# Optimization experiments

Hardware: AMD Instinct MI355X
Metric: run time of the kernel (lower is better)

Reference implementation:

```python
import jax, jax.numpy as jnp
import numpy as np

N_NODES = 10000
N_EDGES = 640000
N_GRAPHS = 64
IN_FEAT = 128
HID = (128, 128)
NUM_CLASS = 10


def setup_inputs() -> dict:
    key = jax.random.key(0)
    ks = jax.random.split(key, 10)
    x = jax.random.normal(ks[0], (N_NODES, IN_FEAT), dtype=jnp.float32)
    edge_index = jax.random.randint(ks[1], (2, N_EDGES), 0, N_NODES, dtype=jnp.int64)
    batch = jnp.sort(jax.random.randint(ks[2], (N_NODES,), 0, N_GRAPHS, dtype=jnp.int64))
    # GCNConv weights (PyG applies x @ W then propagates, bias added after aggregation)
    s1 = 1.0 / np.sqrt(IN_FEAT)
    s2 = 1.0 / np.sqrt(HID[0])
    s3 = 1.0 / np.sqrt(HID[1])
    W1 = jax.random.uniform(ks[3], (IN_FEAT, HID[0]), jnp.float32, -s1, s1)
    b1 = jnp.zeros((HID[0],), jnp.float32)
    W2 = jax.random.uniform(ks[4], (HID[0], HID[1]), jnp.float32, -s2, s2)
    b2 = jnp.zeros((HID[1],), jnp.float32)
    Wlin = jax.random.uniform(ks[5], (HID[1], NUM_CLASS), jnp.float32, -s3, s3)
    blin = jax.random.uniform(ks[6], (NUM_CLASS,), jnp.float32, -s3, s3)
    return {"x": x, "edge_index": edge_index, "batch": batch,
            "W1": W1, "b1": b1, "W2": W2, "b2": b2, "Wlin": Wlin, "blin": blin}


def _gcn_conv(x, src, dst, W, b):
    # GCNConv with self-loops and symmetric normalization:
    # out[i] = sum_{(j->i) in E} d[j]^{-1/2} d[i]^{-1/2} (x_j W) + d[i]^{-1} (x_i W) + b
    # where d = in-degree (on dst) + 1 for the self-loop.
    h = x @ W                                                      # [N, F]
    ones = jnp.ones(src.shape[0], dtype=h.dtype)
    deg = jax.ops.segment_sum(ones, dst, num_segments=x.shape[0]) + 1.0
    dinv = jax.lax.rsqrt(deg)                                      # [N]
    norm = dinv[src] * dinv[dst]                                   # [E]
    agg = jax.ops.segment_sum(h[src] * norm[:, None], dst, num_segments=x.shape[0])
    agg = agg + h * (dinv * dinv)[:, None]                         # self-loop term
    return agg + b


def _global_mean_pool(x, batch, num_graphs):
    sums = jax.ops.segment_sum(x, batch, num_segments=num_graphs)          # [G, F]
    cnt = jax.ops.segment_sum(jnp.ones(x.shape[0], x.dtype), batch, num_segments=num_graphs)
    return sums / jnp.maximum(cnt, 1.0)[:, None]


def reference(x, edge_index, batch, W1, b1, W2, b2, Wlin, blin):
    src, dst = edge_index[0], edge_index[1]
    h = jax.nn.relu(_gcn_conv(x, src, dst, W1, b1))
    h = jax.nn.relu(_gcn_conv(h, src, dst, W2, b2))
    g = _global_mean_pool(h, batch, N_GRAPHS)      # [G, hid1]
    return g @ Wlin + blin                          # [G, num_class]
```

## Files before the change

kernel.cpp:

```cpp
#include <hip/hip_runtime.h>
#include <hip/hip_bf16.h>

#define NN 10000
#define NE 640000
#define NG 64
#define NF 128
#define NC 10
#define TMR 16
#define TKC 32
#define NB 250
#define BSZ 40
#define G1 512
#define ECHUNK 1250


__device__ __forceinline__ unsigned short f2bf(float f) {
    unsigned int u = __float_as_uint(f);
    return (unsigned short)((u + 0x7FFF + ((u >> 16) & 1)) >> 16);
}
__device__ __forceinline__ float bf_lo(unsigned int p) {
    return __uint_as_float(p << 16);
}
__device__ __forceinline__ float bf_hi(unsigned int p) {
    return __uint_as_float(p & 0xFFFF0000u);
}

__device__ __forceinline__ void scan_btot(const int* __restrict__ btot,
                                          int* bbs, int* vv, int* wsum) {
    int tid = threadIdx.x, lane = tid & 63, wv = tid >> 6;
    int v = (tid < NB) ? btot[tid] : 0;
    vv[tid] = v;
    int p = v;
    for (int o = 1; o < 64; o <<= 1) {
        int t = __shfl_up(p, o, 64);
        if (lane >= o) p += t;
    }
    if (lane == 63) wsum[wv] = p;
    __syncthreads();
    int off = 0;
#pragma unroll
    for (int j = 0; j < 4; ++j) if (j < wv) off += wsum[j];
    bbs[tid] = p + off - v;
    __syncthreads();
}

__device__ __forceinline__ int detect64(const int* w, long span) {
    int lane = threadIdx.x & 63;
    long e = (long)lane * (span - 1) / 63;
    return (__ballot(w[2 * e + 1] != 0) == 0ULL) ? 1 : 0;
}

__device__ __forceinline__ int ld_idx(const void* p, long i, int is64) {
    return is64 ? (int)((const long long*)p)[i] : ((const int*)p)[i];
}

__global__ __launch_bounds__(256) void k_hist(const void* __restrict__ ei,
                                              int* __restrict__ bh) {
    int is64 = detect64((const int*)ei, NE);
    __shared__ int hist[256];
    int tid = threadIdx.x;
    hist[tid] = 0;
    __syncthreads();
    int e0 = blockIdx.x * ECHUNK, e1 = min(NE, e0 + ECHUNK);
    for (int e = e0 + tid; e < e1; e += 256) {
        int dst = ld_idx(ei, (long)NE + e, is64);
        atomicAdd(&hist[dst / BSZ], 1);
    }
    __syncthreads();
    bh[tid * G1 + blockIdx.x] = hist[tid];
}

__global__ __launch_bounds__(256) void k_bscan1(int* __restrict__ bh,
                                                int* __restrict__ btot) {
    int w = blockIdx.x * 4 + (threadIdx.x >> 6);
    if (w >= NB) return;
    int lane = threadIdx.x & 63;
    int base = w * G1 + lane * 8;
    int vals[8];
    int lsum = 0;
#pragma unroll
    for (int i = 0; i < 8; ++i) { vals[i] = bh[base + i]; lsum += vals[i]; }
    int pref = lsum;
    for (int o = 1; o < 64; o <<= 1) {
        int t = __shfl_up(pref, o, 64);
        if (lane >= o) pref += t;
    }
    int run = pref - lsum;
#pragma unroll
    for (int i = 0; i < 8; ++i) { int v = vals[i]; bh[base + i] = run; run += v; }
    if (lane == 63) btot[w] = run;
}

__global__ __launch_bounds__(256) void k_bucket(const void* __restrict__ ei,
                                                const int* __restrict__ bh,
                                                const int* __restrict__ btot,
                                                int* __restrict__ ebuf) {
    int is64 = detect64((const int*)ei, NE);
    __shared__ int bbs[256], vv[256], wsum[4];
    __shared__ int cur[256];
    int tid = threadIdx.x;
    scan_btot(btot, bbs, vv, wsum);
    if (tid < NB) cur[tid] = bh[tid * G1 + blockIdx.x] + bbs[tid];
    __syncthreads();
    int e0 = blockIdx.x * ECHUNK, e1 = min(NE, e0 + ECHUNK);
    for (int e = e0 + tid; e < e1; e += 256) {
        int dst = ld_idx(ei, (long)NE + e, is64);
        int src = ld_idx(ei, (long)e, is64);
        int b = dst / BSZ;
        int p = atomicAdd(&cur[b], 1);
        ebuf[p] = ((dst - b * BSZ) << 14) | src;
    }
}

__global__ __launch_bounds__(256) void k_csr(const int* __restrict__ ebuf,
                                             const int* __restrict__ btot,
                                             int* __restrict__ coff,
                                             float* __restrict__ dinv,
                                             unsigned short* __restrict__ csrc) {
    __shared__ int bbs[256], vv[256], wsum[4];
    __shared__ int dcount[BSZ];
    __shared__ int dstart[BSZ];
    __shared__ int cur[BSZ];
    int b = blockIdx.x, tid = threadIdx.x;
    scan_btot(btot, bbs, vv, wsum);
    int base = bbs[b], end = base + vv[b];
    if (tid < BSZ) dcount[tid] = 0;
    __syncthreads();
    for (int i = base + tid; i < end; i += 256)
        atomicAdd(&dcount[ebuf[i] >> 14], 1);
    __syncthreads();
    if (tid == 0) {
        int run = 0;
        for (int i = 0; i < BSZ; ++i) {
            dstart[i] = run; cur[i] = base + run; run += dcount[i];
        }
    }
    __syncthreads();
    if (tid < BSZ) {
        coff[b * BSZ + tid] = base + dstart[tid];
        dinv[b * BSZ + tid] = rsqrtf((float)dcount[tid] + 1.0f);
    }
    if (b == NB - 1 && tid == 0) coff[NN] = NE;
    __syncthreads();
    for (int i = base + tid; i < end; i += 256) {
        int pk = ebuf[i];
        int p = atomicAdd(&cur[pk >> 14], 1);
        csrc[p] = (unsigned short)(pk & 16383);
    }
}

__global__ __launch_bounds__(256) void k_gemm(const float* __restrict__ X,
                                              const float* __restrict__ W,
                                              const float* __restrict__ dinv,
                                              unsigned short* __restrict__ Y,
                                              int nrows) {
    __shared__ float sX[TKC * 20];
    __shared__ float sW[32 * 132];
    int tid = threadIdx.x;
    int rg = tid & 7;
    int cg = tid >> 3;
    int m0 = blockIdx.x * TMR;
    float acc[2][4] = {{0.f}};
    for (int kc = 0; kc < NF / TKC; ++kc) {
        int k0 = kc * TKC;
        if (tid < 128) {
            int row = tid >> 3, kq = tid & 7;
            int mm = m0 + row; if (mm > nrows - 1) mm = nrows - 1;
            float4 v = *(const float4*)(X + (size_t)mm * NF + k0 + kq * 4);
            sX[(kq * 4 + 0) * 20 + row] = v.x;
            sX[(kq * 4 + 1) * 20 + row] = v.y;
            sX[(kq * 4 + 2) * 20 + row] = v.z;
            sX[(kq * 4 + 3) * 20 + row] = v.w;
        }
#pragma unroll
        for (int j = 0; j < 4; ++j) {
            int idx = tid + 256 * j;
            int k = idx >> 5, cq = idx & 31;
            float4 v = *(const float4*)(W + (size_t)(k0 + k) * NF + cq * 4);
            *(float4*)(sW + cq * 132 + k * 4) = v;
        }
        __syncthreads();
#pragma unroll 8
        for (int k = 0; k < TKC; ++k) {
            float2 xf = *(const float2*)(sX + k * 20 + rg * 2);
            float4 wf = *(const float4*)(sW + cg * 132 + k * 4);
            acc[0][0] = fmaf(xf.x, wf.x, acc[0][0]);
            acc[0][1] = fmaf(xf.x, wf.y, acc[0][1]);
            acc[0][2] = fmaf(xf.x, wf.z, acc[0][2]);
            acc[0][3] = fmaf(xf.x, wf.w, acc[0][3]);
            acc[1][0] = fmaf(xf.y, wf.x, acc[1][0]);
            acc[1][1] = fmaf(xf.y, wf.y, acc[1][1]);
            acc[1][2] = fmaf(xf.y, wf.z, acc[1][2]);
            acc[1][3] = fmaf(xf.y, wf.w, acc[1][3]);
        }
        __syncthreads();
    }
#pragma unroll
    for (int r = 0; r < 2; ++r) {
        int m = m0 + rg * 2 + r;
        if (m < nrows) {
            float ds = dinv[m];
            ushort4 h;
            h.x = f2bf(acc[r][0] * ds);
            h.y = f2bf(acc[r][1] * ds);
            h.z = f2bf(acc[r][2] * ds);
            h.w = f2bf(acc[r][3] * ds);
            *(ushort4*)(Y + (size_t)m * NF + cg * 4) = h;
        }
    }
}

__global__ __launch_bounds__(256) void k_gather(const unsigned short* __restrict__ G,
                                                const int* __restrict__ off,
                                                const unsigned short* __restrict__ csrc,
                                                const float* __restrict__ dinv,
                                                const float* __restrict__ bias,
                                                float* __restrict__ OUT) {
    int wid = threadIdx.x >> 6, lane = threadIdx.x & 63;
    int q = lane >> 4, f = lane & 15;
    int n = blockIdx.x * 4 + wid;
    if (n >= NN) return;
    int beg = off[n], end = off[n + 1];
    float din = dinv[n];
    float a0 = 0.f, a1 = 0.f, a2 = 0.f, a3 = 0.f;
    float a4 = 0.f, a5 = 0.f, a6 = 0.f, a7 = 0.f;
    int e = beg + q;
    for (; e + 12 < end; e += 16) {
        int s0 = csrc[e];
        int s1 = csrc[e + 4];
        int s2 = csrc[e + 8];
        int s3 = csrc[e + 12];
        uint4 p0 = ((const uint4*)(G + (size_t)s0 * NF))[f];
        uint4 p1 = ((const uint4*)(G + (size_t)s1 * NF))[f];
        uint4 p2 = ((const uint4*)(G + (size_t)s2 * NF))[f];
        uint4 p3 = ((const uint4*)(G + (size_t)s3 * NF))[f];
        a0 += bf_lo(p0.x); a1 += bf_hi(p0.x); a2 += bf_lo(p0.y); a3 += bf_hi(p0.y);
        a4 += bf_lo(p0.z); a5 += bf_hi(p0.z); a6 += bf_lo(p0.w); a7 += bf_hi(p0.w);
        a0 += bf_lo(p1.x); a1 += bf_hi(p1.x); a2 += bf_lo(p1.y); a3 += bf_hi(p1.y);
        a4 += bf_lo(p1.z); a5 += bf_hi(p1.z); a6 += bf_lo(p1.w); a7 += bf_hi(p1.w);
        a0 += bf_lo(p2.x); a1 += bf_hi(p2.x); a2 += bf_lo(p2.y); a3 += bf_hi(p2.y);
        a4 += bf_lo(p2.z); a5 += bf_hi(p2.z); a6 += bf_lo(p2.w); a7 += bf_hi(p2.w);
        a0 += bf_lo(p3.x); a1 += bf_hi(p3.x); a2 += bf_lo(p3.y); a3 += bf_hi(p3.y);
        a4 += bf_lo(p3.z); a5 += bf_hi(p3.z); a6 += bf_lo(p3.w); a7 += bf_hi(p3.w);
    }
    for (; e < end; e += 4) {
        int s = csrc[e];
        uint4 p = ((const uint4*)(G + (size_t)s * NF))[f];
        a0 += bf_lo(p.x); a1 += bf_hi(p.x); a2 += bf_lo(p.y); a3 += bf_hi(p.y);
        a4 += bf_lo(p.z); a5 += bf_hi(p.z); a6 += bf_lo(p.w); a7 += bf_hi(p.w);
    }
    a0 += __shfl_xor(a0, 16); a1 += __shfl_xor(a1, 16);
    a2 += __shfl_xor(a2, 16); a3 += __shfl_xor(a3, 16);
    a4 += __shfl_xor(a4, 16); a5 += __shfl_xor(a5, 16);
    a6 += __shfl_xor(a6, 16); a7 += __shfl_xor(a7, 16);
    a0 += __shfl_xor(a0, 32); a1 += __shfl_xor(a1, 32);
    a2 += __shfl_xor(a2, 32); a3 += __shfl_xor(a3, 32);
    a4 += __shfl_xor(a4, 32); a5 += __shfl_xor(a5, 32);
    a6 += __shfl_xor(a6, 32); a7 += __shfl_xor(a7, 32);
    if (q == 0) {
        uint4 sp = ((const uint4*)(G + (size_t)n * NF))[f];
        float4 b0 = ((const float4*)bias)[2 * f];
        float4 b1 = ((const float4*)bias)[2 * f + 1];
        float4 o0, o1;
        o0.x = fmaxf(fmaf(din, a0 + bf_lo(sp.x), b0.x), 0.f);
        o0.y = fmaxf(fmaf(din, a1 + bf_hi(sp.x), b0.y), 0.f);
        o0.z = fmaxf(fmaf(din, a2 + bf_lo(sp.y), b0.z), 0.f);
        o0.w = fmaxf(fmaf(din, a3 + bf_hi(sp.y), b0.w), 0.f);
        o1.x = fmaxf(fmaf(din, a4 + bf_lo(sp.z), b1.x), 0.f);
        o1.y = fmaxf(fmaf(din, a5 + bf_hi(sp.z), b1.y), 0.f);
        o1.z = fmaxf(fmaf(din, a6 + bf_lo(sp.w), b1.z), 0.f);
        o1.w = fmaxf(fmaf(din, a7 + bf_hi(sp.w), b1.w), 0.f);
        ((float4*)(OUT + (size_t)n * NF))[2 * f] = o0;
        ((float4*)(OUT + (size_t)n * NF))[2 * f + 1] = o1;
    }
}

__global__ __launch_bounds__(256) void k_poolfin(const float* __restrict__ H,
                                                 const void* __restrict__ batch,
                                                 const float* __restrict__ Wl,
                                                 const float* __restrict__ bl,
                                                 float* __restrict__ out) {
    int is64 = detect64((const int*)batch, NN / 2);
    __shared__ int sb[2];
    __shared__ float4 part[256];
    __shared__ float pooled[NF];
    int g = blockIdx.x;
    int tid = threadIdx.x;
    if (tid < 2) {
        int target = g + tid;
        int lo = 0, hi = NN;
        while (lo < hi) {
            int mid = (lo + hi) >> 1;
            if (ld_idx(batch, mid, is64) < target) lo = mid + 1; else hi = mid;
        }
        sb[tid] = lo;
    }
    __syncthreads();
    int beg = sb[0], end = sb[1];
    int c4 = tid & 31, r = tid >> 5;
    float4 acc = make_float4(0.f, 0.f, 0.f, 0.f);
    for (int n = beg + r; n < end; n += 8) {
        float4 v = ((const float4*)(H + (size_t)n * NF))[c4];
        acc.x += v.x; acc.y += v.y; acc.z += v.z; acc.w += v.w;
    }
    part[tid] = acc;
    __syncthreads();
    if (tid < 32) {
        float4 s = part[tid];
#pragma unroll
        for (int j = 1; j < 8; j++) {
            float4 p = part[tid + 32 * j];
            s.x += p.x; s.y += p.y; s.z += p.z; s.w += p.w;
        }
        float ic = 1.0f / fmaxf((float)(end - beg), 1.0f);
        pooled[tid * 4 + 0] = s.x * ic;
        pooled[tid * 4 + 1] = s.y * ic;
        pooled[tid * 4 + 2] = s.z * ic;
        pooled[tid * 4 + 3] = s.w * ic;
    }
    __syncthreads();
    if (tid < NC) {
        float a = bl[tid];
#pragma unroll 8
        for (int k = 0; k < NF; k++)
            a = fmaf(pooled[k], Wl[k * NC + tid], a);
        out[g * NC + tid] = a;
    }
}

extern "C" void kernel_launch(void* const* d_in, const int* in_sizes, int n_in,
                              void* d_out, int out_size, void* d_ws, size_t ws_size,
                              hipStream_t stream) {
    const float* x  = (const float*)d_in[0];
    const void*  ei = d_in[1];
    const void*  bt = d_in[2];
    const float* W1 = (const float*)d_in[3];
    const float* b1 = (const float*)d_in[4];
    const float* W2 = (const float*)d_in[5];
    const float* b2 = (const float*)d_in[6];
    const float* Wl = (const float*)d_in[7];
    const float* bl = (const float*)d_in[8];

    char* ws = (char*)d_ws;
    int*            coff  = (int*)(ws + 0);
    int*            btot  = (int*)(ws + 40016);
    float*          dinv  = (float*)(ws + 41040);
    unsigned short* csrc  = (unsigned short*)(ws + 81040);
    unsigned short* Gb    = (unsigned short*)(ws + 1361040);
    float*          bufB  = (float*)(ws + 3921040);
    int*            bh    = (int*)(ws + 1361040);
    int*            ebuf  = (int*)(ws + 3921040);

    k_hist  <<<G1, 256, 0, stream>>>(ei, bh);
    k_bscan1<<<(NB + 3) / 4, 256, 0, stream>>>(bh, btot);
    k_bucket<<<G1, 256, 0, stream>>>(ei, bh, btot, ebuf);
    k_csr   <<<NB, 256, 0, stream>>>(ebuf, btot, coff, dinv, csrc);

    k_gemm<<<(NN + TMR - 1) / TMR, 256, 0, stream>>>(x, W1, dinv, Gb, NN);
    k_gather<<<(NN + 3) / 4, 256, 0, stream>>>(Gb, coff, csrc, dinv, b1, bufB);
    k_gemm<<<(NN + TMR - 1) / TMR, 256, 0, stream>>>(bufB, W2, dinv, Gb, NN);
    k_gather<<<(NN + 3) / 4, 256, 0, stream>>>(Gb, coff, csrc, dinv, b2, bufB);

    k_poolfin<<<NG, 256, 0, stream>>>(bufB, bt, Wl, bl, (float*)d_out);
}
```

Baseline: 163.8 us.

## Fuse layer-1 gather with layer-2 GEMM and stage CSR build in LDS

```diff
diff --git a/kernel.cpp b/kernel.cpp
--- a/kernel.cpp
+++ b/kernel.cpp
@@ -12,6 +12,7 @@
 #define BSZ 40
 #define G1 512
 #define ECHUNK 1250
+#define CSRCAP 3072
 
 
 __device__ __forceinline__ unsigned short f2bf(float f) {
@@ -118,21 +119,33 @@
                                              float* __restrict__ dinv,
                                              unsigned short* __restrict__ csrc) {
     __shared__ int bbs[256], vv[256], wsum[4];
+    __shared__ int s[CSRCAP];
+    __shared__ unsigned short t[CSRCAP];
     __shared__ int dcount[BSZ];
     __shared__ int dstart[BSZ];
     __shared__ int cur[BSZ];
     int b = blockIdx.x, tid = threadIdx.x;
     scan_btot(btot, bbs, vv, wsum);
-    int base = bbs[b], end = base + vv[b];
+    int base = bbs[b], cnt = vv[b], end = base + cnt;
     if (tid < BSZ) dcount[tid] = 0;
     __syncthreads();
-    for (int i = base + tid; i < end; i += 256)
-        atomicAdd(&dcount[ebuf[i] >> 14], 1);
+    bool lds = (cnt <= CSRCAP);
+    if (lds) {
+        for (int i = tid; i < cnt; i += 256) s[i] = ebuf[base + i];
+        __syncthreads();
+        for (int i = tid; i < cnt; i += 256)
+            atomicAdd(&dcount[s[i] >> 14], 1);
+    } else {
+        for (int i = base + tid; i < end; i += 256)
+            atomicAdd(&dcount[ebuf[i] >> 14], 1);
+    }
     __syncthreads();
     if (tid == 0) {
         int run = 0;
         for (int i = 0; i < BSZ; ++i) {
-            dstart[i] = run; cur[i] = base + run; run += dcount[i];
+            dstart[i] = run;
+            cur[i] = (lds ? 0 : base) + run;
+            run += dcount[i];
         }
     }
     __syncthreads();
@@ -142,10 +155,20 @@
     }
     if (b == NB - 1 && tid == 0) coff[NN] = NE;
     __syncthreads();
-    for (int i = base + tid; i < end; i += 256) {
-        int pk = ebuf[i];
-        int p = atomicAdd(&cur[pk >> 14], 1);
-        csrc[p] = (unsigned short)(pk & 16383);
+    if (lds) {
+        for (int i = tid; i < cnt; i += 256) {
+            int pk = s[i];
+            int p = atomicAdd(&cur[pk >> 14], 1);
+            t[p] = (unsigned short)(pk & 16383);
+        }
+        __syncthreads();
+        for (int i = tid; i < cnt; i += 256) csrc[base + i] = t[i];
+    } else {
+        for (int i = base + tid; i < end; i += 256) {
+            int pk = ebuf[i];
+            int p = atomicAdd(&cur[pk >> 14], 1);
+            csrc[p] = (unsigned short)(pk & 16383);
+        }
     }
 }
 
@@ -207,6 +230,124 @@
             h.w = f2bf(acc[r][3] * ds);
             *(ushort4*)(Y + (size_t)m * NF + cg * 4) = h;
         }
+    }
+}
+
+__global__ __launch_bounds__(256) void k_gathmm(const unsigned short* __restrict__ G,
+                                                const int* __restrict__ off,
+                                                const unsigned short* __restrict__ csrc,
+                                                const float* __restrict__ dinv,
+                                                const float* __restrict__ b1,
+                                                const float* __restrict__ W2,
+                                                unsigned short* __restrict__ Gb2) {
+    __shared__ float sXT[NF * 18];
+    __shared__ float sW[32 * 132];
+    int tid = threadIdx.x;
+    int wid = tid >> 6, lane = tid & 63;
+    int q = lane >> 4, f = lane & 15;
+    int m0 = blockIdx.x * TMR;
+    for (int tnode = 0; tnode < 4; ++tnode) {
+        int mloc = wid * 4 + tnode;
+        int n = m0 + mloc;
+        int beg = off[n], end = off[n + 1];
+        float din = dinv[n];
+        float a0 = 0.f, a1 = 0.f, a2 = 0.f, a3 = 0.f;
+        float a4 = 0.f, a5 = 0.f, a6 = 0.f, a7 = 0.f;
+        int e = beg + q;
+        for (; e + 12 < end; e += 16) {
+            int s0 = csrc[e];
+            int s1 = csrc[e + 4];
+            int s2 = csrc[e + 8];
+            int s3 = csrc[e + 12];
+            uint4 p0 = ((const uint4*)(G + (size_t)s0 * NF))[f];
+            uint4 p1 = ((const uint4*)(G + (size_t)s1 * NF))[f];
+            uint4 p2 = ((const uint4*)(G + (size_t)s2 * NF))[f];
+            uint4 p3 = ((const uint4*)(G + (size_t)s3 * NF))[f];
+            a0 += bf_lo(p0.x); a1 += bf_hi(p0.x); a2 += bf_lo(p0.y); a3 += bf_hi(p0.y);
+            a4 += bf_lo(p0.z); a5 += bf_hi(p0.z); a6 += bf_lo(p0.w); a7 += bf_hi(p0.w);
+            a0 += bf_lo(p1.x); a1 += bf_hi(p1.x); a2 += bf_lo(p1.y); a3 += bf_hi(p1.y);
+            a4 += bf_lo(p1.z); a5 += bf_hi(p1.z); a6 += bf_lo(p1.w); a7 += bf_hi(p1.w);
+            a0 += bf_lo(p2.x); a1 += bf_hi(p2.x); a2 += bf_lo(p2.y); a3 += bf_hi(p2.y);
+            a4 += bf_lo(p2.z); a5 += bf_hi(p2.z); a6 += bf_lo(p2.w); a7 += bf_hi(p2.w);
+            a0 += bf_lo(p3.x); a1 += bf_hi(p3.x); a2 += bf_lo(p3.y); a3 += bf_hi(p3.y);
+            a4 += bf_lo(p3.z); a5 += bf_hi(p3.z); a6 += bf_lo(p3.w); a7 += bf_hi(p3.w);
+        }
+        for (; e < end; e += 4) {
+            int s = csrc[e];
+            uint4 p = ((const uint4*)(G + (size_t)s * NF))[f];
+            a0 += bf_lo(p.x); a1 += bf_hi(p.x); a2 += bf_lo(p.y); a3 += bf_hi(p.y);
+            a4 += bf_lo(p.z); a5 += bf_hi(p.z); a6 += bf_lo(p.w); a7 += bf_hi(p.w);
+        }
+        a0 += __shfl_xor(a0, 16); a1 += __shfl_xor(a1, 16);
+        a2 += __shfl_xor(a2, 16); a3 += __shfl_xor(a3, 16);
+        a4 += __shfl_xor(a4, 16); a5 += __shfl_xor(a5, 16);
+        a6 += __shfl_xor(a6, 16); a7 += __shfl_xor(a7, 16);
+        a0 += __shfl_xor(a0, 32); a1 += __shfl_xor(a1, 32);
+        a2 += __shfl_xor(a2, 32); a3 += __shfl_xor(a3, 32);
+        a4 += __shfl_xor(a4, 32); a5 += __shfl_xor(a5, 32);
+        a6 += __shfl_xor(a6, 32); a7 += __shfl_xor(a7, 32);
+        if (q == 0) {
+            uint4 sp = ((const uint4*)(G + (size_t)n * NF))[f];
+            float4 c0 = ((const float4*)b1)[2 * f];
+            float4 c1 = ((const float4*)b1)[2 * f + 1];
+            float h0 = fmaxf(fmaf(din, a0 + bf_lo(sp.x), c0.x), 0.f);
+            float h1 = fmaxf(fmaf(din, a1 + bf_hi(sp.x), c0.y), 0.f);
+            float h2 = fmaxf(fmaf(din, a2 + bf_lo(sp.y), c0.z), 0.f);
+            float h3 = fmaxf(fmaf(din, a3 + bf_hi(sp.y), c0.w), 0.f);
+            float h4 = fmaxf(fmaf(din, a4 + bf_lo(sp.z), c1.x), 0.f);
+            float h5 = fmaxf(fmaf(din, a5 + bf_hi(sp.z), c1.y), 0.f);
+            float h6 = fmaxf(fmaf(din, a6 + bf_lo(sp.w), c1.z), 0.f);
+            float h7 = fmaxf(fmaf(din, a7 + bf_hi(sp.w), c1.w), 0.f);
+            int kb = f * 8;
+            sXT[(kb + 0) * 18 + mloc] = h0;
+            sXT[(kb + 1) * 18 + mloc] = h1;
+            sXT[(kb + 2) * 18 + mloc] = h2;
+            sXT[(kb + 3) * 18 + mloc] = h3;
+            sXT[(kb + 4) * 18 + mloc] = h4;
+            sXT[(kb + 5) * 18 + mloc] = h5;
+            sXT[(kb + 6) * 18 + mloc] = h6;
+            sXT[(kb + 7) * 18 + mloc] = h7;
+        }
+    }
+    __syncthreads();
+    int rg = tid & 7;
+    int cg = tid >> 3;
+    float acc[2][4] = {{0.f}};
+    for (int kc = 0; kc < NF / TKC; ++kc) {
+        int k0 = kc * TKC;
+#pragma unroll
+        for (int j = 0; j < 4; ++j) {
+            int idx = tid + 256 * j;
+            int k = idx >> 5, cq = idx & 31;
+            float4 v = *(const float4*)(W2 + (size_t)(k0 + k) * NF + cq * 4);
+            *(float4*)(sW + cq * 132 + k * 4) = v;
+        }
+        __syncthreads();
+#pragma unroll 8
+        for (int k = 0; k < TKC; ++k) {
+            float2 xf = *(const float2*)(sXT + (k0 + k) * 18 + rg * 2);
+            float4 wf = *(const float4*)(sW + cg * 132 + k * 4);
+            acc[0][0] = fmaf(xf.x, wf.x, acc[0][0]);
+            acc[0][1] = fmaf(xf.x, wf.y, acc[0][1]);
+            acc[0][2] = fmaf(xf.x, wf.z, acc[0][2]);
+            acc[0][3] = fmaf(xf.x, wf.w, acc[0][3]);
+            acc[1][0] = fmaf(xf.y, wf.x, acc[1][0]);
+            acc[1][1] = fmaf(xf.y, wf.y, acc[1][1]);
+            acc[1][2] = fmaf(xf.y, wf.z, acc[1][2]);
+            acc[1][3] = fmaf(xf.y, wf.w, acc[1][3]);
+        }
+        __syncthreads();
+    }
+#pragma unroll
+    for (int r = 0; r < 2; ++r) {
+        int m = m0 + rg * 2 + r;
+        float ds = dinv[m];
+        ushort4 h;
+        h.x = f2bf(acc[r][0] * ds);
+        h.y = f2bf(acc[r][1] * ds);
+        h.z = f2bf(acc[r][2] * ds);
+        h.w = f2bf(acc[r][3] * ds);
+        *(ushort4*)(Gb2 + (size_t)m * NF + cg * 4) = h;
     }
 }
 
@@ -346,8 +487,9 @@
     int*            btot  = (int*)(ws + 40016);
     float*          dinv  = (float*)(ws + 41040);
     unsigned short* csrc  = (unsigned short*)(ws + 81040);
-    unsigned short* Gb    = (unsigned short*)(ws + 1361040);
-    float*          bufB  = (float*)(ws + 3921040);
+    unsigned short* Gb1   = (unsigned short*)(ws + 1361040);
+    unsigned short* Gb2   = (unsigned short*)(ws + 3921040);
+    float*          bufB  = (float*)(ws + 6481040);
     int*            bh    = (int*)(ws + 1361040);
     int*            ebuf  = (int*)(ws + 3921040);
 
@@ -356,10 +498,9 @@
     k_bucket<<<G1, 256, 0, stream>>>(ei, bh, btot, ebuf);
     k_csr   <<<NB, 256, 0, stream>>>(ebuf, btot, coff, dinv, csrc);
 
-    k_gemm<<<(NN + TMR - 1) / TMR, 256, 0, stream>>>(x, W1, dinv, Gb, NN);
-    k_gather<<<(NN + 3) / 4, 256, 0, stream>>>(Gb, coff, csrc, dinv, b1, bufB);
-    k_gemm<<<(NN + TMR - 1) / TMR, 256, 0, stream>>>(bufB, W2, dinv, Gb, NN);
-    k_gather<<<(NN + 3) / 4, 256, 0, stream>>>(Gb, coff, csrc, dinv, b2, bufB);
+    k_gemm  <<<(NN + TMR - 1) / TMR, 256, 0, stream>>>(x, W1, dinv, Gb1, NN);
+    k_gathmm<<<NN / TMR, 256, 0, stream>>>(Gb1, coff, csrc, dinv, b1, W2, Gb2);
+    k_gather<<<(NN + 3) / 4, 256, 0, stream>>>(Gb2, coff, csrc, dinv, b2, bufB);
 
     k_poolfin<<<NG, 256, 0, stream>>>(bufB, bt, Wl, bl, (float*)d_out);
 }
```

After: 165.1 us. No clear change (+0.8%).
